# Kernel optimization log

Measured on AMD Instinct MI355X. Metric: run time of the kernel, lower is better.

Reference implementation:

```python
import jax, jax.numpy as jnp
import numpy as np

L, D, H, DH, S, B, V = 8, 1024, 16, 64, 1024, 4, 32000
EPS = 1e-5


def layernorm(x, s, b):
    m = x.mean(-1, keepdims=True)
    v = ((x - m) ** 2).mean(-1, keepdims=True)
    return (x - m) * jax.lax.rsqrt(v + EPS) * s + b


def setup_inputs() -> dict:
    key = jax.random.key(0)
    ks = jax.random.split(key, 12)
    sd = 0.02
    inp = {
        'idx': jax.random.randint(ks[0], (B, S), 0, V),
        'tok_emb': jax.random.normal(ks[1], (V, D), jnp.float32) * sd,
        'pos_emb': jax.random.normal(ks[2], (S, D), jnp.float32) * sd,
        'ln1_s': jnp.ones((L, D), jnp.float32),
        'ln1_b': jnp.zeros((L, D), jnp.float32),
        'wq': jax.random.normal(ks[3], (L, H, D, DH), jnp.float32) * sd,
        'wk': jax.random.normal(ks[4], (L, H, D, DH), jnp.float32) * sd,
        'wv': jax.random.normal(ks[5], (L, H, D, DH), jnp.float32) * sd,
        'wproj': jax.random.normal(ks[6], (L, D, D), jnp.float32) * sd,  # stored [D_in, D_out]
        'ln2_s': jnp.ones((L, D), jnp.float32),
        'ln2_b': jnp.zeros((L, D), jnp.float32),
        'w1': jax.random.normal(ks[7], (L, D, 4 * D), jnp.float32) * sd,
        'b1': jnp.zeros((L, 4 * D), jnp.float32),
        'w2': jax.random.normal(ks[8], (L, 4 * D, D), jnp.float32) * sd,
        'b2': jnp.zeros((L, D), jnp.float32),
        'lnf_s': jnp.ones((D,), jnp.float32),
        'lnf_b': jnp.zeros((D,), jnp.float32),
        'lm_w': jax.random.normal(ks[9], (D, V), jnp.float32) * sd,  # stored [D_in, V]
        'lm_b': jnp.zeros((V,), jnp.float32),
    }
    return inp


def reference(idx, tok_emb, pos_emb, ln1_s, ln1_b, wq, wk, wv, wproj,
              ln2_s, ln2_b, w1, b1, w2, b2, lnf_s, lnf_b, lm_w, lm_b):
    T = idx.shape[1]
    x = tok_emb[idx] + pos_emb[:T]  # [B,T,D]
    mask = jnp.tril(jnp.ones((T, T), bool))
    scale = DH ** -0.5
    for l in range(L):  # fixed small layer count
        h = layernorm(x, ln1_s[l], ln1_b[l])
        q = jnp.einsum('bsd,hde->bhse', h, wq[l])
        k = jnp.einsum('bsd,hde->bhse', h, wk[l])
        v = jnp.einsum('bsd,hde->bhse', h, wv[l])
        att = jnp.einsum('bhse,bhte->bhst', q, k) * scale
        att = jnp.where(mask, att, -jnp.inf)
        att = jax.nn.softmax(att, axis=-1)  # dropout=0.0 -> identity
        o = jnp.einsum('bhst,bhte->bhse', att, v)
        o = o.transpose(0, 2, 1, 3).reshape(x.shape)  # concat heads: [B,T,H*DH]
        x = x + o @ wproj[l]
        h2 = layernorm(x, ln2_s[l], ln2_b[l])
        x = x + jax.nn.relu(h2 @ w1[l] + b1[l]) @ w2[l] + b2[l]
    x = layernorm(x, lnf_s, lnf_b)
    logits = x @ lm_w + lm_b  # [B,T,V]
    return logits
```

## Files before the change

### kernel.cpp

```cpp
#include <hip/hip_runtime.h>
#include <hip/hip_bf16.h>

#define LL 8
#define DD 1024
#define HH 16
#define DHH 64
#define SS 1024
#define BB 4
#define VV 32000
#define MM (BB * SS)

typedef unsigned short u16;
typedef __attribute__((ext_vector_type(8))) short short8v;
typedef __attribute__((ext_vector_type(4))) float f32x4;
typedef unsigned int __attribute__((address_space(1))) guint;
typedef unsigned int __attribute__((address_space(3))) luint;

__device__ __forceinline__ float bf2f_lo(unsigned u) { return __uint_as_float(u << 16); }
__device__ __forceinline__ u16 f2bf(float f) {
  unsigned x = __float_as_uint(f);
  return (u16)((x + 0x7fffu + ((x >> 16) & 1u)) >> 16);
}

__global__ __launch_bounds__(256) void embed_kernel(
    const int* __restrict__ idx, const float* __restrict__ tok,
    const float* __restrict__ pos, float* __restrict__ x) {
  int i = blockIdx.x * blockDim.x + threadIdx.x;
  int elem = i * 4;
  int row = elem / DD;
  int d = elem % DD;
  int s = row % SS;
  int t = idx[row];
  float4 tv = *(const float4*)(tok + (size_t)t * DD + d);
  float4 pv = *(const float4*)(pos + (size_t)s * DD + d);
  tv.x += pv.x; tv.y += pv.y; tv.z += pv.z; tv.w += pv.w;
  *(float4*)(x + (size_t)elem) = tv;
}

__global__ __launch_bounds__(256) void ln_bf16_kernel(
    const float* __restrict__ x, const float* __restrict__ sc,
    const float* __restrict__ bi, u16* __restrict__ out) {
  const int row = blockIdx.x;
  const int tid = threadIdx.x;
  __shared__ float red[4];
  float4 v = ((const float4*)(x + (size_t)row * DD))[tid];
  float s = v.x + v.y + v.z + v.w;
  #pragma unroll
  for (int off = 32; off; off >>= 1) s += __shfl_down(s, off);
  if ((tid & 63) == 0) red[tid >> 6] = s;
  __syncthreads();
  float mean = (red[0] + red[1] + red[2] + red[3]) * (1.f / DD);
  float dx = v.x - mean, dy = v.y - mean, dz = v.z - mean, dw = v.w - mean;
  float vs = dx * dx + dy * dy + dz * dz + dw * dw;
  __syncthreads();
  #pragma unroll
  for (int off = 32; off; off >>= 1) vs += __shfl_down(vs, off);
  if ((tid & 63) == 0) red[tid >> 6] = vs;
  __syncthreads();
  float var = (red[0] + red[1] + red[2] + red[3]) * (1.f / DD);
  float rstd = rsqrtf(var + 1e-5f);
  float4 s4 = ((const float4*)sc)[tid];
  float4 b4 = ((const float4*)bi)[tid];
  ushort4 o;
  o.x = f2bf(dx * rstd * s4.x + b4.x);
  o.y = f2bf(dy * rstd * s4.y + b4.y);
  o.z = f2bf(dz * rstd * s4.z + b4.z);
  o.w = f2bf(dw * rstd * s4.w + b4.w);
  *(ushort4*)(out + (size_t)row * DD + tid * 4) = o;
}

template <bool HEADW>
__global__ __launch_bounds__(256) void convT_kernel(
    const float* __restrict__ W, u16* __restrict__ BT, int K, int N,
    size_t lstride) {
  __shared__ float tile[32][33];
  const int n0 = blockIdx.x * 32, k0 = blockIdx.y * 32, l = blockIdx.z;
  const int tx = threadIdx.x & 31, ty = threadIdx.x >> 5;
  const float* Wl;
  int ld;
  if (HEADW) {
    const int h = n0 >> 6;
    Wl = W + ((size_t)(l * HH + h) * K) * 64 + (n0 & 63);
    ld = 64;
  } else {
    Wl = W + (size_t)l * K * N + n0;
    ld = N;
  }
  #pragma unroll
  for (int i = 0; i < 4; ++i)
    tile[ty + 8 * i][tx] = Wl[(size_t)(k0 + ty + 8 * i) * ld + tx];
  __syncthreads();
  u16* out = BT + (size_t)l * lstride;
  #pragma unroll
  for (int i = 0; i < 4; ++i)
    out[(size_t)(n0 + ty + 8 * i) * K + k0 + tx] = f2bf(tile[tx][ty + 8 * i]);
}

__global__ __launch_bounds__(256) void transpose_v(
    const u16* __restrict__ qkv, u16* __restrict__ vt) {
  __shared__ u16 t[32][33];
  const int s0 = blockIdx.x * 32, d0 = blockIdx.y * 32;
  const int tx = threadIdx.x & 31, ty = threadIdx.x >> 5;
  #pragma unroll
  for (int i = 0; i < 4; ++i)
    t[ty + 8 * i][tx] = qkv[(size_t)(s0 + ty + 8 * i) * 3072 + 2048 + d0 + tx];
  __syncthreads();
  #pragma unroll
  for (int i = 0; i < 4; ++i)
    vt[(size_t)(d0 + ty + 8 * i) * MM + s0 + tx] = t[tx][ty + 8 * i];
}

#define BARRIER __builtin_amdgcn_s_barrier()
#define MEMFENCE asm volatile("" ::: "memory")
#define MROW(F, AQ, B0,B1,B2,B3) \
  acc[F][0] = __builtin_amdgcn_mfma_f32_16x16x32_bf16(AQ, B0, acc[F][0], 0, 0, 0); \
  acc[F][1] = __builtin_amdgcn_mfma_f32_16x16x32_bf16(AQ, B1, acc[F][1], 0, 0, 0); \
  acc[F][2] = __builtin_amdgcn_mfma_f32_16x16x32_bf16(AQ, B2, acc[F][2], 0, 0, 0); \
  acc[F][3] = __builtin_amdgcn_mfma_f32_16x16x32_bf16(AQ, B3, acc[F][3], 0, 0, 0);

#define LDA_(BUF, KH, F) \
  (*(const short8v*)&As[BUF][KH][(wm * 128 + (F) * 16 + (lane & 15)) * 32 + rg])
#define LDB_(BUF, KH, NF) \
  (*(const short8v*)&Bs[BUF][KH][(wn * 64 + (NF) * 16 + (lane & 15)) * 32 + rg])
#define LDS_A(S0,S1,S2,S3, BUF, KH, FB) { \
  S0 = LDA_(BUF, KH, (FB) + 0); S1 = LDA_(BUF, KH, (FB) + 1); \
  S2 = LDA_(BUF, KH, (FB) + 2); S3 = LDA_(BUF, KH, (FB) + 3); }
#define LDS_B(S0,S1,S2,S3, BUF, KH) { \
  S0 = LDB_(BUF, KH, 0); S1 = LDB_(BUF, KH, 1); \
  S2 = LDB_(BUF, KH, 2); S3 = LDB_(BUF, KH, 3); }
#define STAGE_A(BUF, KH, KT) do { \
  __builtin_amdgcn_global_load_lds((const guint*)(Abase + (KT) * 64 + (KH) * 32), \
      (luint*)(&As[BUF][KH][tid * 8]), 16, 0, 0); \
  __builtin_amdgcn_global_load_lds((const guint*)(Abase + (size_t)128 * K + (KT) * 64 + (KH) * 32), \
      (luint*)(&As[BUF][KH][(tid + 512) * 8]), 16, 0, 0); \
} while (0)
#define STAGE_B(BUF, KH, KT) do { \
  __builtin_amdgcn_global_load_lds((const guint*)(Bbase + (KT) * 64 + (KH) * 32), \
      (luint*)(&Bs[BUF][KH][tid * 8]), 16, 0, 0); \
  __builtin_amdgcn_global_load_lds((const guint*)(Bbase + (size_t)128 * K + (KT) * 64 + (KH) * 32), \
      (luint*)(&Bs[BUF][KH][(tid + 512) * 8]), 16, 0, 0); \
} while (0)
#define MFMA16S(FB, A0,A1,A2,A3, B0,B1,B2,B3) \
  MROW((FB) + 0, A0, B0,B1,B2,B3) MROW((FB) + 1, A1, B0,B1,B2,B3) \
  MROW((FB) + 2, A2, B0,B1,B2,B3) MROW((FB) + 3, A3, B0,B1,B2,B3)

#define TILE4(CUR, KT, ST1, ST2, V1STR, V3STR, LD4, LGK4STR) { \
  const int cur_ = (CUR); \
   \
  MEMFENCE; \
  LDS_A(aN0,aN1,aN2,aN3, cur_, 0, 4); \
  if (ST1) { STAGE_A(cur_ ^ 1, 1, (KT) + 1); } \
  asm volatile("s_waitcnt " V1STR ::: "memory"); \
  asm volatile("s_waitcnt lgkmcnt(4)" ::: "memory"); \
  BARRIER; \
  __builtin_amdgcn_s_setprio(1); \
  MFMA16S(0, aP0,aP1,aP2,aP3, bP0,bP1,bP2,bP3); \
  __builtin_amdgcn_s_setprio(0); \
   \
  MEMFENCE; \
  LDS_A(aP0,aP1,aP2,aP3, cur_, 1, 0); \
  LDS_B(bN0,bN1,bN2,bN3, cur_, 1); \
  if (ST1) { STAGE_B(cur_ ^ 1, 1, (KT) + 1); } \
  asm volatile("s_waitcnt lgkmcnt(8)" ::: "memory"); \
  BARRIER; \
  __builtin_amdgcn_s_setprio(1); \
  MFMA16S(4, aN0,aN1,aN2,aN3, bP0,bP1,bP2,bP3); \
  __builtin_amdgcn_s_setprio(0); \
   \
  MEMFENCE; \
  LDS_A(aN0,aN1,aN2,aN3, cur_, 1, 4); \
  if (ST2) { STAGE_A(cur_, 0, (KT) + 2); } \
  asm volatile("s_waitcnt " V3STR ::: "memory"); \
  asm volatile("s_waitcnt lgkmcnt(4)" ::: "memory"); \
  BARRIER; \
  __builtin_amdgcn_s_setprio(1); \
  MFMA16S(0, aP0,aP1,aP2,aP3, bN0,bN1,bN2,bN3); \
  __builtin_amdgcn_s_setprio(0); \
   \
  MEMFENCE; \
  if (LD4) { LDS_A(aP0,aP1,aP2,aP3, cur_ ^ 1, 0, 0); \
             LDS_B(bP0,bP1,bP2,bP3, cur_ ^ 1, 0); } \
  if (ST2) { STAGE_B(cur_, 0, (KT) + 2); } \
  asm volatile("s_waitcnt " LGK4STR ::: "memory"); \
  BARRIER; \
  __builtin_amdgcn_s_setprio(1); \
  MFMA16S(4, aN0,aN1,aN2,aN3, bN0,bN1,bN2,bN3); \
  __builtin_amdgcn_s_setprio(0); \
}

template <bool BIAS, bool RELU, bool RESID, bool OBF16>
__global__ __launch_bounds__(512, 2) void gemm8(
    const u16* __restrict__ A, const u16* __restrict__ BT,
    const float* __restrict__ bias, const float* __restrict__ resid,
    void* __restrict__ Cv, int M, int N, int K) {
  __shared__ u16 As[2][2][8192];
  __shared__ u16 Bs[2][2][8192];
  const int tid = threadIdx.x;
  const int lane = tid & 63, wave = tid >> 6;
  const int wm = wave >> 2, wn = wave & 3;
  const int nwg = gridDim.x;
  const int bid = blockIdx.x;
  const int wg = ((nwg & 7) == 0) ? ((bid & 7) * (nwg >> 3) + (bid >> 3)) : bid;
  const int nmt = M >> 8;
  const int m0 = (wg % nmt) * 256;
  const int n0 = (wg / nmt) * 256;
  const int NT = K >> 6;
  const int sr = tid >> 2;
  const int ssc = (((tid & 3) ^ ((tid >> 3) & 3)) * 8);
  const u16* Abase = A + (size_t)(m0 + sr) * K + ssc;
  const u16* Bbase = BT + (size_t)(n0 + sr) * K + ssc;
  const int rg = (((lane >> 4) ^ ((lane >> 1) & 3)) * 8);

  f32x4 acc[8][4] = {};
  short8v aP0, aP1, aP2, aP3, aN0, aN1, aN2, aN3;
  short8v bP0, bP1, bP2, bP3, bN0, bN1, bN2, bN3;

  STAGE_A(0, 0, 0); STAGE_B(0, 0, 0);
  STAGE_A(0, 1, 0); STAGE_B(0, 1, 0);
  STAGE_A(1, 0, 1); STAGE_B(1, 0, 1);
  asm volatile("s_waitcnt vmcnt(8)" ::: "memory");
  BARRIER;
  MEMFENCE;
  LDS_A(aP0,aP1,aP2,aP3, 0, 0, 0);
  LDS_B(bP0,bP1,bP2,bP3, 0, 0);

  int kt = 0;
  for (; kt < NT - 2; ++kt) {
    TILE4(kt & 1, kt, true, true, "vmcnt(6)", "vmcnt(6)", true, "lgkmcnt(8)");
  }
  TILE4(kt & 1, kt, true, false, "vmcnt(6)", "vmcnt(4)", true, "lgkmcnt(8)");
  ++kt;
  TILE4(kt & 1, kt, false, false, "vmcnt(0)", "vmcnt(0)", false, "lgkmcnt(0)");

  #pragma unroll
  for (int f = 0; f < 8; ++f) {
    #pragma unroll
    for (int n = 0; n < 4; ++n) {
      const int col = n0 + wn * 64 + n * 16 + (lane & 15);
      #pragma unroll
      for (int r = 0; r < 4; ++r) {
        const int row = m0 + wm * 128 + f * 16 + (lane >> 4) * 4 + r;
        float v = acc[f][n][r];
        if (BIAS) v += bias[col];
        if (RELU) v = fmaxf(v, 0.f);
        if (RESID) v += resid[(size_t)row * N + col];
        if (OBF16)
          ((u16*)Cv)[(size_t)row * N + col] = f2bf(v);
        else
          ((float*)Cv)[(size_t)row * N + col] = v;
      }
    }
  }
}

#define LDA4_(BUF, KH, F) \
  (*(const short8v*)&As[BUF][KH][(wm * 64 + (F) * 16 + (lane & 15)) * 32 + rg])
#define LDB4_(BUF, KH, NF) \
  (*(const short8v*)&Bs[BUF][KH][(wn * 64 + (NF) * 16 + (lane & 15)) * 32 + rg])
#define STAGE_A4(BUF, KH, KT) do { \
  __builtin_amdgcn_global_load_lds((const guint*)(Abase + (KT) * 64 + (KH) * 32), \
      (luint*)(&As[BUF][KH][tid * 8]), 16, 0, 0); \
  __builtin_amdgcn_global_load_lds((const guint*)(Abase + (size_t)64 * K + (KT) * 64 + (KH) * 32), \
      (luint*)(&As[BUF][KH][(tid + 256) * 8]), 16, 0, 0); \
} while (0)
#define STAGE_B4(BUF, KH, KT) do { \
  __builtin_amdgcn_global_load_lds((const guint*)(Bbase + (KT) * 64 + (KH) * 32), \
      (luint*)(&Bs[BUF][KH][tid * 8]), 16, 0, 0); \
  __builtin_amdgcn_global_load_lds((const guint*)(Bbase + (size_t)64 * K + (KT) * 64 + (KH) * 32), \
      (luint*)(&Bs[BUF][KH][(tid + 256) * 8]), 16, 0, 0); \
} while (0)
#define MFMA8S(F0, F1, A0, A1, B0,B1,B2,B3) \
  MROW(F0, A0, B0,B1,B2,B3) MROW(F1, A1, B0,B1,B2,B3)

#define TILE4P(CUR, KT, ST1, ST2, V1STR, V3STR, LD4, LGK4STR) { \
  const int cur_ = (CUR); \
  MEMFENCE; \
  aN0 = LDA4_(cur_, 0, 2); aN1 = LDA4_(cur_, 0, 3); \
  if (ST1) { STAGE_A4(cur_ ^ 1, 1, (KT) + 1); } \
  asm volatile("s_waitcnt " V1STR ::: "memory"); \
  asm volatile("s_waitcnt lgkmcnt(2)" ::: "memory"); \
  BARRIER; \
  __builtin_amdgcn_s_setprio(1); \
  MFMA8S(0, 1, aP0, aP1, bP0,bP1,bP2,bP3); \
  __builtin_amdgcn_s_setprio(0); \
  MEMFENCE; \
  aP0 = LDA4_(cur_, 1, 0); aP1 = LDA4_(cur_, 1, 1); \
  bN0 = LDB4_(cur_, 1, 0); bN1 = LDB4_(cur_, 1, 1); \
  bN2 = LDB4_(cur_, 1, 2); bN3 = LDB4_(cur_, 1, 3); \
  if (ST1) { STAGE_B4(cur_ ^ 1, 1, (KT) + 1); } \
  asm volatile("s_waitcnt lgkmcnt(6)" ::: "memory"); \
  BARRIER; \
  __builtin_amdgcn_s_setprio(1); \
  MFMA8S(2, 3, aN0, aN1, bP0,bP1,bP2,bP3); \
  __builtin_amdgcn_s_setprio(0); \
  MEMFENCE; \
  aN0 = LDA4_(cur_, 1, 2); aN1 = LDA4_(cur_, 1, 3); \
  if (ST2) { STAGE_A4(cur_, 0, (KT) + 2); } \
  asm volatile("s_waitcnt " V3STR ::: "memory"); \
  asm volatile("s_waitcnt lgkmcnt(2)" ::: "memory"); \
  BARRIER; \
  __builtin_amdgcn_s_setprio(1); \
  MFMA8S(0, 1, aP0, aP1, bN0,bN1,bN2,bN3); \
  __builtin_amdgcn_s_setprio(0); \
  MEMFENCE; \
  if (LD4) { aP0 = LDA4_(cur_ ^ 1, 0, 0); aP1 = LDA4_(cur_ ^ 1, 0, 1); \
             bP0 = LDB4_(cur_ ^ 1, 0, 0); bP1 = LDB4_(cur_ ^ 1, 0, 1); \
             bP2 = LDB4_(cur_ ^ 1, 0, 2); bP3 = LDB4_(cur_ ^ 1, 0, 3); } \
  if (ST2) { STAGE_B4(cur_, 0, (KT) + 2); } \
  asm volatile("s_waitcnt " LGK4STR ::: "memory"); \
  BARRIER; \
  __builtin_amdgcn_s_setprio(1); \
  MFMA8S(2, 3, aN0, aN1, bN0,bN1,bN2,bN3); \
  __builtin_amdgcn_s_setprio(0); \
}

template <bool BIAS, bool RELU, bool RESID, bool OBF16>
__global__ __launch_bounds__(256, 2) void gemm4p(
    const u16* __restrict__ A, const u16* __restrict__ BT,
    const float* __restrict__ bias, const float* __restrict__ resid,
    void* __restrict__ Cv, int M, int N, int K) {
  __shared__ u16 As[2][2][4096];
  __shared__ u16 Bs[2][2][4096];
  const int tid = threadIdx.x;
  const int lane = tid & 63, wave = tid >> 6;
  const int wm = wave >> 1, wn = wave & 1;
  const int m0 = blockIdx.x * 128, n0 = blockIdx.y * 128;
  const int NT = K >> 6;
  const int sr = tid >> 2;
  const int ssc = (((tid & 3) ^ ((tid >> 3) & 3)) * 8);
  const u16* Abase = A + (size_t)(m0 + sr) * K + ssc;
  const u16* Bbase = BT + (size_t)(n0 + sr) * K + ssc;
  const int rg = (((lane >> 4) ^ ((lane >> 1) & 3)) * 8);

  f32x4 acc[4][4] = {};
  short8v aP0, aP1, aN0, aN1;
  short8v bP0, bP1, bP2, bP3, bN0, bN1, bN2, bN3;

  STAGE_A4(0, 0, 0); STAGE_B4(0, 0, 0);
  STAGE_A4(0, 1, 0); STAGE_B4(0, 1, 0);
  STAGE_A4(1, 0, 1); STAGE_B4(1, 0, 1);
  asm volatile("s_waitcnt vmcnt(8)" ::: "memory");
  BARRIER;
  MEMFENCE;
  aP0 = LDA4_(0, 0, 0); aP1 = LDA4_(0, 0, 1);
  bP0 = LDB4_(0, 0, 0); bP1 = LDB4_(0, 0, 1);
  bP2 = LDB4_(0, 0, 2); bP3 = LDB4_(0, 0, 3);

  int kt = 0;
  for (; kt < NT - 2; ++kt) {
    TILE4P(kt & 1, kt, true, true, "vmcnt(6)", "vmcnt(6)", true, "lgkmcnt(6)");
  }
  TILE4P(kt & 1, kt, true, false, "vmcnt(6)", "vmcnt(4)", true, "lgkmcnt(6)");
  ++kt;
  TILE4P(kt & 1, kt, false, false, "vmcnt(0)", "vmcnt(0)", false, "lgkmcnt(0)");

  #pragma unroll
  for (int f = 0; f < 4; ++f) {
    #pragma unroll
    for (int n = 0; n < 4; ++n) {
      const int col = n0 + wn * 64 + n * 16 + (lane & 15);
      #pragma unroll
      for (int r = 0; r < 4; ++r) {
        const int row = m0 + wm * 64 + f * 16 + (lane >> 4) * 4 + r;
        float v = acc[f][n][r];
        if (BIAS) v += bias[col];
        if (RELU) v = fmaxf(v, 0.f);
        if (RESID) v += resid[(size_t)row * N + col];
        if (OBF16)
          ((u16*)Cv)[(size_t)row * N + col] = f2bf(v);
        else
          ((float*)Cv)[(size_t)row * N + col] = v;
      }
    }
  }
}

__global__ __launch_bounds__(256) void gemm_fb(
    const u16* __restrict__ A, const float* __restrict__ B,
    const float* __restrict__ bias, float* __restrict__ C, int M, int N, int K) {
  __shared__ alignas(16) float Asm[16][68];
  __shared__ alignas(16) float Bsm[16][68];
  const int tid = threadIdx.x;
  const int tx = tid & 15, ty = tid >> 4;
  const int m0 = blockIdx.y * 64, n0 = blockIdx.x * 64;
  const int ar = tid >> 2, ac = (tid & 3) * 4;
  const int br = tid >> 4, bc = (tid & 15) * 4;
  float acc[4][4] = {};
  for (int k0 = 0; k0 < K; k0 += 16) {
    ushort4 au = *(const ushort4*)(A + (size_t)(m0 + ar) * K + k0 + ac);
    float4 bv = *(const float4*)(B + (size_t)(k0 + br) * N + n0 + bc);
    Asm[ac + 0][ar] = bf2f_lo(au.x);
    Asm[ac + 1][ar] = bf2f_lo(au.y);
    Asm[ac + 2][ar] = bf2f_lo(au.z);
    Asm[ac + 3][ar] = bf2f_lo(au.w);
    *(float4*)&Bsm[br][bc] = bv;
    __syncthreads();
    #pragma unroll
    for (int kk = 0; kk < 16; ++kk) {
      float4 a = *(const float4*)&Asm[kk][ty * 4];
      float4 b = *(const float4*)&Bsm[kk][tx * 4];
      acc[0][0] += a.x * b.x; acc[0][1] += a.x * b.y; acc[0][2] += a.x * b.z; acc[0][3] += a.x * b.w;
      acc[1][0] += a.y * b.x; acc[1][1] += a.y * b.y; acc[1][2] += a.y * b.z; acc[1][3] += a.y * b.w;
      acc[2][0] += a.z * b.x; acc[2][1] += a.z * b.y; acc[2][2] += a.z * b.z; acc[2][3] += a.z * b.w;
      acc[3][0] += a.w * b.x; acc[3][1] += a.w * b.y; acc[3][2] += a.w * b.z; acc[3][3] += a.w * b.w;
    }
    __syncthreads();
  }
  #pragma unroll
  for (int i = 0; i < 4; ++i) {
    const int m = m0 + ty * 4 + i;
    #pragma unroll
    for (int j = 0; j < 4; ++j) {
      const int n = n0 + tx * 4 + j;
      C[(size_t)m * N + n] = acc[i][j] + bias[n];
    }
  }
}

__global__ __launch_bounds__(512) void attn_mfma(
    const u16* __restrict__ qkv, const u16* __restrict__ vt,
    u16* __restrict__ o) {
  __shared__ alignas(16) u16 Ksh[64 * 64];
  __shared__ alignas(16) u16 Vsh[64 * 64];
  __shared__ unsigned Plds[8][16 * 41];
  __shared__ float bcast[8][16];
  const int tid = threadIdx.x;
  const int lane = tid & 63, wave = tid >> 6;
  const int g = lane >> 4, qi = lane & 15;
  const int qt = (SS / 128 - 1) - blockIdx.x;
  const int h = blockIdx.y, b = blockIdx.z;
  const int q0w = qt * 128 + wave * 16;
  const int ktmax = 2 * qt + 1;

  short8v qf0, qf1;
  {
    const u16* qp = qkv + ((size_t)b * SS + q0w + qi) * 3072 + h * DHH + g * 8;
    qf0 = *(const short8v*)qp;
    qf1 = *(const short8v*)(qp + 32);
  }

  f32x4 oacc[4] = {};
  float mrow = -1e30f, lrow = 0.f;

  for (int kt = 0; kt <= ktmax; ++kt) {
    __syncthreads();
    {
      const int row = tid >> 3, ch = tid & 7;
      const int sch = ch ^ (row & 7);
      __builtin_amdgcn_global_load_lds(
          (const guint*)(qkv + ((size_t)b * SS + kt * 64 + row) * 3072 + 1024 + h * DHH + sch * 8),
          (luint*)(Ksh + tid * 8), 16, 0, 0);
      __builtin_amdgcn_global_load_lds(
          (const guint*)(vt + ((size_t)(h * DHH + row)) * MM + b * SS + kt * 64 + sch * 8),
          (luint*)(Vsh + tid * 8), 16, 0, 0);
    }
    __syncthreads();

    const bool active = (kt * 64 <= q0w + 15);
    if (active) {
      f32x4 st[4] = {};
      #pragma unroll
      for (int t = 0; t < 4; ++t) {
        const int row = t * 16 + qi;
        const int swz = (row & 7) << 4;
        short8v kf0 = *(const short8v*)(Ksh + row * 64 + (((g * 16) ^ swz) >> 1));
        short8v kf1 = *(const short8v*)(Ksh + row * 64 + (((64 + g * 16) ^ swz) >> 1));
        st[t] = __builtin_amdgcn_mfma_f32_16x16x32_bf16(kf0, qf0, st[t], 0, 0, 0);
        st[t] = __builtin_amdgcn_mfma_f32_16x16x32_bf16(kf1, qf1, st[t], 0, 0, 0);
      }

      const int diag = q0w + qi - kt * 64;
      if (diag < 63) {
        #pragma unroll
        for (int t = 0; t < 4; ++t)
          #pragma unroll
          for (int r = 0; r < 4; ++r)
            if (t * 16 + 4 * g + r > diag) st[t][r] = -1e30f;
      }

      float mt = st[0][0];
      #pragma unroll
      for (int t = 0; t < 4; ++t)
        #pragma unroll
        for (int r = 0; r < 4; ++r) mt = fmaxf(mt, st[t][r]);
      mt = fmaxf(mt, __shfl_xor(mt, 16));
      mt = fmaxf(mt, __shfl_xor(mt, 32));
      const float mnew = fmaxf(mrow, mt * 0.125f);
      const float corr = __expf(mrow - mnew);
      float pl = 0.f;
      #pragma unroll
      for (int t = 0; t < 4; ++t) {
        #pragma unroll
        for (int r2 = 0; r2 < 2; ++r2) {
          float plo = __expf(fmaf(st[t][2 * r2], 0.125f, -mnew));
          float phi = __expf(fmaf(st[t][2 * r2 + 1], 0.125f, -mnew));
          pl += plo + phi;
          Plds[wave][qi * 41 + 8 * t + 2 * g + r2] =
              (unsigned)f2bf(plo) | ((unsigned)f2bf(phi) << 16);
        }
      }
      pl += __shfl_xor(pl, 16);
      pl += __shfl_xor(pl, 32);
      lrow = lrow * corr + pl;
      mrow = mnew;

      if (g == 0) bcast[wave][qi] = corr;
      float c0 = bcast[wave][g * 4 + 0];
      float c1 = bcast[wave][g * 4 + 1];
      float c2 = bcast[wave][g * 4 + 2];
      float c3 = bcast[wave][g * 4 + 3];
      #pragma unroll
      for (int dvt = 0; dvt < 4; ++dvt) {
        oacc[dvt][0] *= c0; oacc[dvt][1] *= c1;
        oacc[dvt][2] *= c2; oacc[dvt][3] *= c3;
      }

      union U8 { unsigned u[4]; short8v s8; };
      U8 pa0, pa1;
      #pragma unroll
      for (int c = 0; c < 4; ++c) {
        pa0.u[c] = Plds[wave][qi * 41 + g * 4 + c];
        pa1.u[c] = Plds[wave][qi * 41 + 16 + g * 4 + c];
      }
      #pragma unroll
      for (int dvt = 0; dvt < 4; ++dvt) {
        const int row = dvt * 16 + qi;
        const int swz = (row & 7) << 4;
        short8v v0 = *(const short8v*)(Vsh + row * 64 + (((g * 16) ^ swz) >> 1));
        short8v v1 = *(const short8v*)(Vsh + row * 64 + (((64 + g * 16) ^ swz) >> 1));
        oacc[dvt] = __builtin_amdgcn_mfma_f32_16x16x32_bf16(pa0.s8, v0, oacc[dvt], 0, 0, 0);
        oacc[dvt] = __builtin_amdgcn_mfma_f32_16x16x32_bf16(pa1.s8, v1, oacc[dvt], 0, 0, 0);
      }
    }
  }

  if (g == 0) bcast[wave][qi] = 1.f / lrow;
  float i0 = bcast[wave][g * 4 + 0];
  float i1 = bcast[wave][g * 4 + 1];
  float i2 = bcast[wave][g * 4 + 2];
  float i3 = bcast[wave][g * 4 + 3];
  #pragma unroll
  for (int dvt = 0; dvt < 4; ++dvt) {
    const int col = h * DHH + dvt * 16 + qi;
    o[((size_t)b * SS + q0w + g * 4 + 0) * DD + col] = f2bf(oacc[dvt][0] * i0);
    o[((size_t)b * SS + q0w + g * 4 + 1) * DD + col] = f2bf(oacc[dvt][1] * i1);
    o[((size_t)b * SS + q0w + g * 4 + 2) * DD + col] = f2bf(oacc[dvt][2] * i2);
    o[((size_t)b * SS + q0w + g * 4 + 3) * DD + col] = f2bf(oacc[dvt][3] * i3);
  }
}

extern "C" void kernel_launch(void* const* d_in, const int* in_sizes, int n_in,
                              void* d_out, int out_size, void* d_ws, size_t ws_size,
                              hipStream_t stream) {
  const int* idx = (const int*)d_in[0];
  const float* tok_emb = (const float*)d_in[1];
  const float* pos_emb = (const float*)d_in[2];
  const float* ln1_s = (const float*)d_in[3];
  const float* ln1_b = (const float*)d_in[4];
  const float* wq = (const float*)d_in[5];
  const float* wk = (const float*)d_in[6];
  const float* wv = (const float*)d_in[7];
  const float* wproj = (const float*)d_in[8];
  const float* ln2_s = (const float*)d_in[9];
  const float* ln2_b = (const float*)d_in[10];
  const float* w1 = (const float*)d_in[11];
  const float* b1 = (const float*)d_in[12];
  const float* w2 = (const float*)d_in[13];
  const float* b2 = (const float*)d_in[14];
  const float* lnf_s = (const float*)d_in[15];
  const float* lnf_b = (const float*)d_in[16];
  const float* lm_w = (const float*)d_in[17];
  const float* lm_b = (const float*)d_in[18];

  const size_t MD = (size_t)MM * DD;

  u16* sc0 = (u16*)d_out;
  u16* BTqkv = sc0;
  u16* BTp = BTqkv + (size_t)LL * 3072 * DD;
  u16* BTw1 = BTp + (size_t)LL * DD * DD;
  u16* BTw2 = BTw1 + (size_t)LL * DD * 4 * DD;
  u16* qkvb = BTw2 + (size_t)LL * DD * 4 * DD;
  u16* vtb = qkvb + (size_t)MM * 3072;
  u16* ob = vtb + MD;
  u16* tmp = ob + MD;

  float* x = (float*)d_ws;
  u16* h = (u16*)((char*)d_ws + MD * 4);
  u16* BTlm = (u16*)((char*)d_ws + MD * 4 + MD * 2);
  const bool big_ws = ws_size >= (MD * 4 + MD * 2 + (size_t)VV * DD * 2);

  const dim3 blk(256);

  convT_kernel<true><<<dim3(DD / 32, DD / 32, LL), blk, 0, stream>>>(
      wq, BTqkv, DD, DD, (size_t)3072 * DD);
  convT_kernel<true><<<dim3(DD / 32, DD / 32, LL), blk, 0, stream>>>(
      wk, BTqkv + (size_t)DD * DD, DD, DD, (size_t)3072 * DD);
  convT_kernel<true><<<dim3(DD / 32, DD / 32, LL), blk, 0, stream>>>(
      wv, BTqkv + (size_t)2 * DD * DD, DD, DD, (size_t)3072 * DD);
  convT_kernel<false><<<dim3(DD / 32, DD / 32, LL), blk, 0, stream>>>(
      wproj, BTp, DD, DD, (size_t)DD * DD);
  convT_kernel<false><<<dim3(4 * DD / 32, DD / 32, LL), blk, 0, stream>>>(
      w1, BTw1, DD, 4 * DD, (size_t)DD * 4 * DD);
  convT_kernel<false><<<dim3(DD / 32, 4 * DD / 32, LL), blk, 0, stream>>>(
      w2, BTw2, 4 * DD, DD, (size_t)4 * DD * DD);
  if (big_ws)
    convT_kernel<false><<<dim3(VV / 32, DD / 32, 1), blk, 0, stream>>>(
        lm_w, BTlm, DD, VV, (size_t)VV * DD);

  embed_kernel<<<(MM * DD / 4 + 255) / 256, blk, 0, stream>>>(idx, tok_emb, pos_emb, x);

  for (int l = 0; l < LL; ++l) {
    ln_bf16_kernel<<<MM, blk, 0, stream>>>(x, ln1_s + l * DD, ln1_b + l * DD, h);
    gemm8<false, false, false, true><<<dim3((MM / 256) * (3072 / 256)), dim3(512), 0, stream>>>(
        h, BTqkv + (size_t)l * 3072 * DD, nullptr, nullptr, qkvb, MM, 3072, DD);
    transpose_v<<<dim3(MM / 32, DD / 32), blk, 0, stream>>>(qkvb, vtb);
    attn_mfma<<<dim3(SS / 128, HH, BB), dim3(512), 0, stream>>>(qkvb, vtb, ob);
    gemm4p<false, false, true, false><<<dim3(MM / 128, DD / 128), blk, 0, stream>>>(
        ob, BTp + (size_t)l * DD * DD, nullptr, x, x, MM, DD, DD);
    ln_bf16_kernel<<<MM, blk, 0, stream>>>(x, ln2_s + l * DD, ln2_b + l * DD, h);
    gemm8<true, true, false, true><<<dim3((MM / 256) * (4 * DD / 256)), dim3(512), 0, stream>>>(
        h, BTw1 + (size_t)l * DD * 4 * DD, b1 + (size_t)l * 4 * DD, nullptr, tmp,
        MM, 4 * DD, DD);
    gemm4p<true, false, true, false><<<dim3(MM / 128, DD / 128), blk, 0, stream>>>(
        tmp, BTw2 + (size_t)l * 4 * DD * DD, b2 + (size_t)l * DD, x, x, MM, DD, 4 * DD);
  }

  ln_bf16_kernel<<<MM, blk, 0, stream>>>(x, lnf_s, lnf_b, h);
  if (big_ws) {
    gemm8<true, false, false, false><<<dim3((MM / 256) * (VV / 256)), dim3(512), 0, stream>>>(
        h, BTlm, lm_b, nullptr, (float*)d_out, MM, VV, DD);
  } else {
    gemm_fb<<<dim3(VV / 64, MM / 64), blk, 0, stream>>>(
        h, lm_w, lm_b, (float*)d_out, MM, VV, DD);
  }
}
```

Baseline: 2.392 ms.

## Compute V transposed directly via swapped-operand GEMM, drop transpose kernel

Splits the fused QKV projection into a QK projection and a separate V projection computed as Wv^T·h^T, so V comes out already transposed in the layout the attention kernel reads. This removes the per-layer transpose_v kernel and its extra global read and write of V. In exchange the single large 256-tile gemm8 launch becomes two gemm4p launches with 128 tiles, which may use the matrix units less efficiently than the bigger tiles.

```diff
diff --git a/kernel.cpp b/kernel.cpp
--- a/kernel.cpp
+++ b/kernel.cpp
@@ -94,20 +94,6 @@
   #pragma unroll
   for (int i = 0; i < 4; ++i)
     out[(size_t)(n0 + ty + 8 * i) * K + k0 + tx] = f2bf(tile[tx][ty + 8 * i]);
-}
-
-__global__ __launch_bounds__(256) void transpose_v(
-    const u16* __restrict__ qkv, u16* __restrict__ vt) {
-  __shared__ u16 t[32][33];
-  const int s0 = blockIdx.x * 32, d0 = blockIdx.y * 32;
-  const int tx = threadIdx.x & 31, ty = threadIdx.x >> 5;
-  #pragma unroll
-  for (int i = 0; i < 4; ++i)
-    t[ty + 8 * i][tx] = qkv[(size_t)(s0 + ty + 8 * i) * 3072 + 2048 + d0 + tx];
-  __syncthreads();
-  #pragma unroll
-  for (int i = 0; i < 4; ++i)
-    vt[(size_t)(d0 + ty + 8 * i) * MM + s0 + tx] = t[tx][ty + 8 * i];
 }
 
 #define BARRIER __builtin_amdgcn_s_barrier()
@@ -418,7 +404,7 @@
 }
 
 __global__ __launch_bounds__(512) void attn_mfma(
-    const u16* __restrict__ qkv, const u16* __restrict__ vt,
+    const u16* __restrict__ qk, const u16* __restrict__ vt,
     u16* __restrict__ o) {
   __shared__ alignas(16) u16 Ksh[64 * 64];
   __shared__ alignas(16) u16 Vsh[64 * 64];
@@ -434,7 +420,7 @@
 
   short8v qf0, qf1;
   {
-    const u16* qp = qkv + ((size_t)b * SS + q0w + qi) * 3072 + h * DHH + g * 8;
+    const u16* qp = qk + ((size_t)b * SS + q0w + qi) * 2048 + h * DHH + g * 8;
     qf0 = *(const short8v*)qp;
     qf1 = *(const short8v*)(qp + 32);
   }
@@ -448,7 +434,7 @@
       const int row = tid >> 3, ch = tid & 7;
       const int sch = ch ^ (row & 7);
       __builtin_amdgcn_global_load_lds(
-          (const guint*)(qkv + ((size_t)b * SS + kt * 64 + row) * 3072 + 1024 + h * DHH + sch * 8),
+          (const guint*)(qk + ((size_t)b * SS + kt * 64 + row) * 2048 + 1024 + h * DHH + sch * 8),
           (luint*)(Ksh + tid * 8), 16, 0, 0);
       __builtin_amdgcn_global_load_lds(
           (const guint*)(vt + ((size_t)(h * DHH + row)) * MM + b * SS + kt * 64 + sch * 8),
@@ -575,12 +561,13 @@
   const size_t MD = (size_t)MM * DD;
 
   u16* sc0 = (u16*)d_out;
-  u16* BTqkv = sc0;
-  u16* BTp = BTqkv + (size_t)LL * 3072 * DD;
+  u16* BTqk = sc0;
+  u16* BTv = BTqk + (size_t)LL * 2048 * DD;
+  u16* BTp = BTv + (size_t)LL * DD * DD;
   u16* BTw1 = BTp + (size_t)LL * DD * DD;
   u16* BTw2 = BTw1 + (size_t)LL * DD * 4 * DD;
-  u16* qkvb = BTw2 + (size_t)LL * DD * 4 * DD;
-  u16* vtb = qkvb + (size_t)MM * 3072;
+  u16* qkb = BTw2 + (size_t)LL * DD * 4 * DD;
+  u16* vtb = qkb + (size_t)MM * 2048;
   u16* ob = vtb + MD;
   u16* tmp = ob + MD;
 
@@ -592,11 +579,11 @@
   const dim3 blk(256);
 
   convT_kernel<true><<<dim3(DD / 32, DD / 32, LL), blk, 0, stream>>>(
-      wq, BTqkv, DD, DD, (size_t)3072 * DD);
+      wq, BTqk, DD, DD, (size_t)2048 * DD);
   convT_kernel<true><<<dim3(DD / 32, DD / 32, LL), blk, 0, stream>>>(
-      wk, BTqkv + (size_t)DD * DD, DD, DD, (size_t)3072 * DD);
+      wk, BTqk + (size_t)DD * DD, DD, DD, (size_t)2048 * DD);
   convT_kernel<true><<<dim3(DD / 32, DD / 32, LL), blk, 0, stream>>>(
-      wv, BTqkv + (size_t)2 * DD * DD, DD, DD, (size_t)3072 * DD);
+      wv, BTv, DD, DD, (size_t)DD * DD);
   convT_kernel<false><<<dim3(DD / 32, DD / 32, LL), blk, 0, stream>>>(
       wproj, BTp, DD, DD, (size_t)DD * DD);
   convT_kernel<false><<<dim3(4 * DD / 32, DD / 32, LL), blk, 0, stream>>>(
@@ -611,10 +598,11 @@
 
   for (int l = 0; l < LL; ++l) {
     ln_bf16_kernel<<<MM, blk, 0, stream>>>(x, ln1_s + l * DD, ln1_b + l * DD, h);
-    gemm8<false, false, false, true><<<dim3((MM / 256) * (3072 / 256)), dim3(512), 0, stream>>>(
-        h, BTqkv + (size_t)l * 3072 * DD, nullptr, nullptr, qkvb, MM, 3072, DD);
-    transpose_v<<<dim3(MM / 32, DD / 32), blk, 0, stream>>>(qkvb, vtb);
-    attn_mfma<<<dim3(SS / 128, HH, BB), dim3(512), 0, stream>>>(qkvb, vtb, ob);
+    gemm4p<false, false, false, true><<<dim3(MM / 128, 2048 / 128), blk, 0, stream>>>(
+        h, BTqk + (size_t)l * 2048 * DD, nullptr, nullptr, qkb, MM, 2048, DD);
+    gemm4p<false, false, false, true><<<dim3(DD / 128, MM / 128), blk, 0, stream>>>(
+        BTv + (size_t)l * DD * DD, h, nullptr, nullptr, vtb, DD, MM, DD);
+    attn_mfma<<<dim3(SS / 128, HH, BB), dim3(512), 0, stream>>>(qkb, vtb, ob);
     gemm4p<false, false, true, false><<<dim3(MM / 128, DD / 128), blk, 0, stream>>>(
         ob, BTp + (size_t)l * DD * DD, nullptr, x, x, MM, DD, DD);
     ln_bf16_kernel<<<MM, blk, 0, stream>>>(x, ln2_s + l * DD, ln2_b + l * DD, h);
```

After: 2.530 ms. +5.8%, slower.
